# Kernel tuning notes

Hardware: AMD Instinct MI355X
Metric: run time of the kernel (lower is better)

## Reference

```python
import jax, jax.numpy as jnp
import numpy as np

N, D, H, DH = 8192, 512, 8, 64          # seq len, model dim, heads, head dim
NF = int(DH * math_log) if False else 266  # nb_features = int(64 * ln(64)) = 266
EPS = 1e-4                               # performer softmax-kernel eps
LN_EPS = 1e-5


def layernorm(x, g, b):
    mu = x.mean(-1, keepdims=True)
    var = ((x - mu) ** 2).mean(-1, keepdims=True)
    return (x - mu) * jax.lax.rsqrt(var + LN_EPS) * g + b


def softmax_kernel(data, proj, is_query):
    # data: [b,h,n,dh], proj: [nf,dh] -> phi(data): [b,h,n,nf]
    dnorm = DH ** -0.25
    ratio = NF ** -0.5
    dd = jnp.einsum('bhnd,jd->bhnj', data * dnorm, proj)
    diag = (data ** 2).sum(-1, keepdims=True) * 0.5 * (dnorm ** 2)
    if is_query:
        m = jnp.max(dd, axis=-1, keepdims=True)
    else:
        m = jnp.max(dd, axis=(-1, -2), keepdims=True)
    return ratio * (jnp.exp(dd - diag - m) + EPS)


def setup_inputs() -> dict:
    key = jax.random.key(0)
    ks = jax.random.split(key, 10)
    s = 0.02
    return {
        'x': jax.random.normal(ks[0], (N, D), jnp.float32),
        'proj': jax.random.normal(ks[1], (NF, DH), jnp.float32),
        'ln1_g': jnp.ones((D,), jnp.float32), 'ln1_b': jnp.zeros((D,), jnp.float32),
        'wq': jax.random.normal(ks[2], (D, D), jnp.float32) * s,
        'wk': jax.random.normal(ks[3], (D, D), jnp.float32) * s,
        'wv': jax.random.normal(ks[4], (D, D), jnp.float32) * s,
        'wo': jax.random.normal(ks[5], (D, D), jnp.float32) * s,
        'wo_b': jnp.zeros((D,), jnp.float32),
        'ln2_g': jnp.ones((D,), jnp.float32), 'ln2_b': jnp.zeros((D,), jnp.float32),
        'w1': jax.random.normal(ks[6], (D, 4 * D), jnp.float32) * s,
        'b1': jnp.zeros((4 * D,), jnp.float32),
        'w2': jax.random.normal(ks[7], (4 * D, D), jnp.float32) * s,
        'b2': jnp.zeros((D,), jnp.float32),
    }


def reference(x, proj, ln1_g, ln1_b, wq, wk, wv, wo, wo_b, ln2_g, ln2_b, w1, b1, w2, b2):
    xb = x[None]                                     # [1,N,D] (the unsqueeze(0))
    # --- PreLN FAVOR+ self-attention ---
    h = layernorm(xb, ln1_g, ln1_b)
    def split_heads(t):
        return t.reshape(1, N, H, DH).transpose(0, 2, 1, 3)   # [1,H,N,DH]
    q = split_heads(h @ wq)
    k = split_heads(h @ wk)
    v = split_heads(h @ wv)
    qp = softmax_kernel(q, proj, True)               # [1,H,N,NF]
    kp = softmax_kernel(k, proj, False)              # [1,H,N,NF]
    # non-causal linear attention
    context = jnp.einsum('bhnj,bhnd->bhjd', kp, v)   # [1,H,NF,DH]
    d_inv = 1.0 / jnp.einsum('bhnj,bhj->bhn', qp, kp.sum(axis=2))
    attn = jnp.einsum('bhnj,bhjd->bhnd', qp, context) * d_inv[..., None]
    attn = attn.transpose(0, 2, 1, 3).reshape(1, N, D)
    xb = xb + attn @ wo + wo_b
    # --- PreLN feed-forward (GELU, mult=4) ---
    h2 = layernorm(xb, ln2_g, ln2_b)
    xb = xb + jax.nn.gelu(h2 @ w1 + b1) @ w2 + b2
    return xb[0]                                     # squeeze -> [N,D]
```

## Files before the change

### kernel.cpp

```cpp
#include <hip/hip_runtime.h>
#include <math.h>


typedef __attribute__((ext_vector_type(8))) short bf16x8;
typedef __attribute__((ext_vector_type(4))) float f32x4;

#define N_SEQ 8192
#define DMODEL 512
#define DQKV 1536
#define NHEAD 8
#define DHEAD 64
#define NF 266
#define NFP 320
#define PEPS 1e-4f
#define LNEPS 1e-5f
#define RATIO 0.06131393694f

__device__ __forceinline__ unsigned short f2bf(float f) {
  unsigned u = __float_as_uint(f);
  u += 0x7FFFu + ((u >> 16) & 1u);
  return (unsigned short)(u >> 16);
}
__device__ __forceinline__ float bf2f(unsigned short b) {
  return __uint_as_float(((unsigned)b) << 16);
}
__device__ __forceinline__ unsigned enc_f32(float f) {
  unsigned i = __float_as_uint(f);
  return (i & 0x80000000u) ? ~i : (i | 0x80000000u);
}
__device__ __forceinline__ float dec_f32(unsigned u) {
  return (u & 0x80000000u) ? __uint_as_float(u & 0x7FFFFFFFu) : __uint_as_float(~u);
}

__device__ __forceinline__ void g2l16(const void* g, void* l) {
  __builtin_amdgcn_global_load_lds(
      (const __attribute__((address_space(1))) void*)g,
      (__attribute__((address_space(3))) void*)l, 16, 0, 0);
}

template <int N>
__device__ __forceinline__ void wait_vmcnt() {
  if constexpr (N == 0) asm volatile("s_waitcnt vmcnt(0)" ::: "memory");
  else if constexpr (N == 8) asm volatile("s_waitcnt vmcnt(8)" ::: "memory");
}
__device__ __forceinline__ void wait_lgkm0() {
  asm volatile("s_waitcnt lgkmcnt(0)" ::: "memory");
}


__global__ __launch_bounds__(256) void prep_kernel(
    const float* __restrict__ wq, const float* __restrict__ wk,
    const float* __restrict__ wv, const float* __restrict__ wo,
    const float* __restrict__ w1, const float* __restrict__ w2,
    const float* __restrict__ proj,
    unsigned short* __restrict__ wtqkv, unsigned short* __restrict__ wot,
    unsigned short* __restrict__ w1t, unsigned short* __restrict__ w2t,
    unsigned short* __restrict__ pb, unsigned* __restrict__ mk) {
  int bid = blockIdx.x;
  if (bid < 3072) {
    const float* src; unsigned short* dst; int R, C, base;
    if (bid < 256)       { src = wq; dst = wtqkv;          R = 512;  C = 512;  base = 0; }
    else if (bid < 512)  { src = wk; dst = wtqkv + 262144; R = 512;  C = 512;  base = 256; }
    else if (bid < 768)  { src = wv; dst = wtqkv + 524288; R = 512;  C = 512;  base = 512; }
    else if (bid < 1024) { src = wo; dst = wot;            R = 512;  C = 512;  base = 768; }
    else if (bid < 2048) { src = w1; dst = w1t;            R = 512;  C = 2048; base = 1024; }
    else                 { src = w2; dst = w2t;            R = 2048; C = 512;  base = 2048; }
    int lb = bid - base;
    int nbx = C / 32;
    int c0 = (lb % nbx) * 32, r0 = (lb / nbx) * 32;
    __shared__ float tile[32][33];
    int tx = threadIdx.x & 31, ty = threadIdx.x >> 5;
    #pragma unroll
    for (int i = ty; i < 32; i += 8)
      tile[i][tx] = src[(long)(r0 + i) * C + c0 + tx];
    __syncthreads();
    #pragma unroll
    for (int i = ty; i < 32; i += 8)
      dst[(long)(c0 + i) * R + r0 + tx] = f2bf(tile[tx][i]);
  } else if (bid < 3152) {
    int id = (bid - 3072) * 256 + threadIdx.x;
    int j = id >> 6;
    pb[id] = (j < NF) ? f2bf(proj[(long)j * 64 + (id & 63)] * 0.35355339059327373f)
                      : (unsigned short)0;
  } else {
    if (threadIdx.x < NHEAD) mk[threadIdx.x] = 0x007FFFFFu;
  }
}


__global__ __launch_bounds__(256) void ln_kernel(const float* __restrict__ x,
                                                 const float* __restrict__ g,
                                                 const float* __restrict__ b,
                                                 unsigned short* __restrict__ out) {
  __shared__ float sred[4];
  int row = blockIdx.x, t = threadIdx.x;
  float2 v = ((const float2*)(x + (long)row * DMODEL))[t];
  float s = v.x + v.y;
  #pragma unroll
  for (int m = 32; m >= 1; m >>= 1) s += __shfl_xor(s, m);
  if ((t & 63) == 0) sred[t >> 6] = s;
  __syncthreads();
  float mu = (sred[0] + sred[1] + sred[2] + sred[3]) * (1.0f / DMODEL);
  __syncthreads();
  float d0 = v.x - mu, d1 = v.y - mu;
  float q = d0 * d0 + d1 * d1;
  #pragma unroll
  for (int m = 32; m >= 1; m >>= 1) q += __shfl_xor(q, m);
  if ((t & 63) == 0) sred[t >> 6] = q;
  __syncthreads();
  float var = (sred[0] + sred[1] + sred[2] + sred[3]) * (1.0f / DMODEL);
  float inv = rsqrtf(var + LNEPS);
  int c = t * 2;
  unsigned short o0 = f2bf(d0 * inv * g[c] + b[c]);
  unsigned short o1 = f2bf(d1 * inv * g[c + 1] + b[c + 1]);
  ((unsigned*)(out + (long)row * DMODEL))[t] = ((unsigned)o1 << 16) | o0;
}

enum { EPI_BF16 = 0, EPI_BIAS_RES_F32 = 2, EPI_BIAS_GELU = 3, EPI_QKV = 4 };


template <int EPI>
__global__ __launch_bounds__(512, 1) void gemm8p_kernel(
    const unsigned short* __restrict__ A, int lda,
    const unsigned short* __restrict__ Bt, int ldb,
    void* __restrict__ Cv, int ldc,
    int K,
    const float* __restrict__ bias,
    unsigned short* __restrict__ vt) {
  constexpr int MR = 8, NR = 4;
  const int tid = threadIdx.x;
  const int wave = tid >> 6, lane = tid & 63;
  const int lr = lane & 15, lg = lane >> 4;
  const int wr = wave >> 2, wc = wave & 3;
  const int m0 = blockIdx.x * 256, n0 = blockIdx.y * 256;

  __shared__ uint4 a_s[2][2048];
  __shared__ uint4 b_s[2][2048];

  const unsigned short* asrc[4];
  const unsigned short* bsrc[4];
  #pragma unroll
  for (int e = 0; e < 4; ++e) {
    int chunk = e * 512 + tid;
    int r = chunk >> 3, c = chunk & 7;
    asrc[e] = A + (long)(m0 + r) * lda + (c ^ (r & 7)) * 8;
    bsrc[e] = Bt + (long)(n0 + r) * ldb + (c ^ (r & 7)) * 8;
  }
  const int wbase = tid & 448;

  f32x4 acc[MR][NR] = {};

  auto stage_a = [&](int buf, int t) {
    #pragma unroll
    for (int e = 0; e < 4; ++e)
      g2l16(asrc[e] + t * 64, &a_s[buf][e * 512 + wbase]);
  };
  auto stage_b = [&](int buf, int t) {
    #pragma unroll
    for (int e = 0; e < 4; ++e)
      g2l16(bsrc[e] + t * 64, &b_s[buf][e * 512 + wbase]);
  };
  auto compute_ks = [&](int buf, int ks) {
    bf16x8 af[MR], bv[NR];
    #pragma unroll
    for (int i = 0; i < MR; ++i) {
      int r = wr * 128 + i * 16 + lr;
      af[i] = *(const bf16x8*)&a_s[buf][r * 8 + ((ks * 4 + lg) ^ (r & 7))];
    }
    #pragma unroll
    for (int j = 0; j < NR; ++j) {
      int r = wc * 64 + j * 16 + lr;
      bv[j] = *(const bf16x8*)&b_s[buf][r * 8 + ((ks * 4 + lg) ^ (r & 7))];
    }
    __builtin_amdgcn_s_setprio(1);
    #pragma unroll
    for (int i = 0; i < MR; ++i)
      #pragma unroll
      for (int j = 0; j < NR; ++j)
        acc[i][j] = __builtin_amdgcn_mfma_f32_16x16x32_bf16(af[i], bv[j], acc[i][j], 0, 0, 0);
    __builtin_amdgcn_s_setprio(0);
  };

  const int NT = K >> 6;
  stage_a(0, 0);
  stage_b(0, 0);
  wait_vmcnt<0>();
  __builtin_amdgcn_s_barrier();

  for (int t = 0; t < NT; ++t) {
    const int cur = t & 1;
    const bool more = (t + 1 < NT);
    if (more) stage_a(cur ^ 1, t + 1);
    compute_ks(cur, 0);
    if (more) stage_b(cur ^ 1, t + 1);
    compute_ks(cur, 1);
    if (more) {
      wait_lgkm0();
      __builtin_amdgcn_sched_barrier(0);
      __builtin_amdgcn_s_barrier();
      wait_vmcnt<0>();
      __builtin_amdgcn_s_barrier();
    }
  }

  #pragma unroll
  for (int i = 0; i < MR; ++i) {
    #pragma unroll
    for (int j = 0; j < NR; ++j) {
      int gn = n0 + wc * 64 + j * 16 + lr;
      int gm0 = m0 + wr * 128 + i * 16 + lg * 4;
      if (EPI == EPI_QKV && gn >= 1024) {
        int d = gn - 1024;
        uint2 u;
        u.x = (unsigned)f2bf(acc[i][j][0]) | ((unsigned)f2bf(acc[i][j][1]) << 16);
        u.y = (unsigned)f2bf(acc[i][j][2]) | ((unsigned)f2bf(acc[i][j][3]) << 16);
        *(uint2*)(vt + (long)d * N_SEQ + gm0) = u;
        continue;
      }
      #pragma unroll
      for (int rg = 0; rg < 4; ++rg) {
        int gm = gm0 + rg;
        float v = acc[i][j][rg];
        if (EPI == EPI_BF16 || EPI == EPI_QKV) {
          ((unsigned short*)Cv)[(long)gm * ldc + gn] = f2bf(v);
        } else if (EPI == EPI_BIAS_GELU) {
          v += bias[gn];
          float t3 = 0.7978845608028654f * (v + 0.044715f * v * v * v);
          v = v / (1.0f + __expf(-2.0f * t3));
          ((unsigned short*)Cv)[(long)gm * ldc + gn] = f2bf(v);
        }
      }
    }
  }
}


template <int BM, int BN, int WM, int WN, int EPI>
__global__ __launch_bounds__(256) void gemm_kernel(
    const unsigned short* __restrict__ A, int lda,
    const unsigned short* __restrict__ Bt, int ldb,
    void* __restrict__ Cv, int ldc,
    int K,
    const float* __restrict__ bias,
    const float* __restrict__ res, int ldr) {
  static_assert((BM / WM) * (BN / WN) == 4, "need 4 waves");
  constexpr int MR = WM / 16, NR = WN / 16;
  constexpr int WNN = BN / WN;
  constexpr int AIT = BM * 8 / 256;
  constexpr int BIT = BN * 8 / 256;
  const int tid = threadIdx.x;
  const int wave = tid >> 6, lane = tid & 63;
  const int lr = lane & 15, lg = lane >> 4;
  const int wr = wave / WNN, wc = wave % WNN;
  const int m0 = blockIdx.x * BM, n0 = blockIdx.y * BN;

  __shared__ uint4 a_s[2][BM * 8];
  __shared__ uint4 b_s[2][BN * 8];

  const unsigned short* asrc[AIT];
  #pragma unroll
  for (int e = 0; e < AIT; ++e) {
    int chunk = e * 256 + tid;
    int r = chunk >> 3, c = chunk & 7;
    asrc[e] = A + (long)(m0 + r) * lda + (c ^ (r & 7)) * 8;
  }
  const unsigned short* bsrc[BIT];
  #pragma unroll
  for (int e = 0; e < BIT; ++e) {
    int chunk = e * 256 + tid;
    int r = chunk >> 3, c = chunk & 7;
    bsrc[e] = Bt + (long)(n0 + r) * ldb + (c ^ (r & 7)) * 8;
  }
  const int wbase = tid & 192;

  f32x4 acc[MR][NR] = {};

  auto stage = [&](int buf, int t) {
    #pragma unroll
    for (int e = 0; e < AIT; ++e)
      g2l16(asrc[e] + t * 64, &a_s[buf][e * 256 + wbase]);
    #pragma unroll
    for (int e = 0; e < BIT; ++e)
      g2l16(bsrc[e] + t * 64, &b_s[buf][e * 256 + wbase]);
  };
  auto compute = [&](int buf) {
    #pragma unroll
    for (int ks = 0; ks < 2; ++ks) {
      bf16x8 af[MR], bv[NR];
      #pragma unroll
      for (int i = 0; i < MR; ++i) {
        int r = wr * WM + i * 16 + lr;
        af[i] = *(const bf16x8*)&a_s[buf][r * 8 + ((ks * 4 + lg) ^ (r & 7))];
      }
      #pragma unroll
      for (int j = 0; j < NR; ++j) {
        int r = wc * WN + j * 16 + lr;
        bv[j] = *(const bf16x8*)&b_s[buf][r * 8 + ((ks * 4 + lg) ^ (r & 7))];
      }
      #pragma unroll
      for (int i = 0; i < MR; ++i)
        #pragma unroll
        for (int j = 0; j < NR; ++j)
          acc[i][j] = __builtin_amdgcn_mfma_f32_16x16x32_bf16(af[i], bv[j], acc[i][j], 0, 0, 0);
    }
  };

  const int NT = K >> 6;
  stage(0, 0);
  stage(1, 1);
  wait_vmcnt<8>();
  __builtin_amdgcn_s_barrier();

  int cur = 0;
  for (int t = 0; t < NT; ++t) {
    compute(cur);
    if (t + 1 < NT) {
      wait_lgkm0();
      __builtin_amdgcn_s_barrier();
      if (t + 2 < NT) {
        stage(cur, t + 2);
        wait_vmcnt<8>();
      } else {
        wait_vmcnt<0>();
      }
      __builtin_amdgcn_s_barrier();
    }
    cur ^= 1;
  }

  #pragma unroll
  for (int i = 0; i < MR; ++i) {
    #pragma unroll
    for (int j = 0; j < NR; ++j) {
      int gn = n0 + wc * WN + j * 16 + lr;
      #pragma unroll
      for (int rg = 0; rg < 4; ++rg) {
        int gm = m0 + wr * WM + i * 16 + lg * 4 + rg;
        float v = acc[i][j][rg];
        if (EPI == EPI_BF16) {
          ((unsigned short*)Cv)[(long)gm * ldc + gn] = f2bf(v);
        } else if (EPI == EPI_BIAS_RES_F32) {
          v += bias[gn] + res[(long)gm * ldr + gn];
          ((float*)Cv)[(long)gm * ldc + gn] = v;
        } else if (EPI == EPI_BIAS_GELU) {
          v += bias[gn];
          float t3 = 0.7978845608028654f * (v + 0.044715f * v * v * v);
          v = v / (1.0f + __expf(-2.0f * t3));
          ((unsigned short*)Cv)[(long)gm * ldc + gn] = f2bf(v);
        }
      }
    }
  }
}


__global__ __launch_bounds__(256) void kmax_kernel(
    const unsigned short* __restrict__ Kp,
    const unsigned short* __restrict__ pb,
    unsigned* __restrict__ mk) {
  const int tid = threadIdx.x;
  const int wave = tid >> 6, lane = tid & 63;
  const int lr = lane & 15, lg = lane >> 4;
  const int h = blockIdx.z;
  const int m0 = blockIdx.x * 64;

  __shared__ uint4 a_s4[512];
  __shared__ uint4 b_s4[2560];
  __shared__ float sred[4];

  const unsigned short* Aq = Kp + (long)m0 * DQKV + h * DHEAD;
  const int wbase = tid & 192;

  #pragma unroll
  for (int e = 0; e < 2; ++e) {
    int chunk = e * 256 + tid;
    int r = chunk >> 3, c = chunk & 7;
    g2l16(Aq + (long)r * DQKV + (c ^ (r & 7)) * 8, a_s4 + e * 256 + wbase);
  }
  #pragma unroll
  for (int e = 0; e < 10; ++e) {
    int chunk = e * 256 + tid;
    int r = chunk >> 3, c = chunk & 7;
    g2l16(pb + (long)r * DHEAD + (c ^ (r & 7)) * 8, b_s4 + e * 256 + wbase);
  }
  __syncthreads();

  f32x4 acc[17] = {};
  #pragma unroll
  for (int ks = 0; ks < 2; ++ks) {
    int rA = wave * 16 + lr;
    bf16x8 af = *(const bf16x8*)&a_s4[rA * 8 + ((ks * 4 + lg) ^ (rA & 7))];
    #pragma unroll
    for (int j = 0; j < 17; ++j) {
      int rB = j * 16 + lr;
      bf16x8 bv = *(const bf16x8*)&b_s4[rB * 8 + ((ks * 4 + lg) ^ (rB & 7))];
      acc[j] = __builtin_amdgcn_mfma_f32_16x16x32_bf16(af, bv, acc[j], 0, 0, 0);
    }
  }

  float m = -3.0e38f;
  #pragma unroll
  for (int j = 0; j < 17; ++j) {
    bool valid = (j < 16) || (lr < 10);
    if (valid) {
      #pragma unroll
      for (int rg = 0; rg < 4; ++rg) m = fmaxf(m, acc[j][rg]);
    }
  }
  #pragma unroll
  for (int s = 1; s < 64; s <<= 1) m = fmaxf(m, __shfl_xor(m, s));
  if (lane == 0) sred[wave] = m;
  __syncthreads();
  if (tid == 0) {
    float mm = fmaxf(fmaxf(sred[0], sred[1]), fmaxf(sred[2], sred[3]));
    atomicMax(&mk[h], enc_f32(mm));
  }
}


__global__ __launch_bounds__(256) void ctx_fused_kernel(
    const unsigned short* __restrict__ Kp,
    const unsigned short* __restrict__ pb,
    const unsigned short* __restrict__ vT,
    const unsigned* __restrict__ mk,
    float* __restrict__ part,
    float* __restrict__ kspart) {
  const int tid = threadIdx.x;
  const int wave = tid >> 6, lane = tid & 63;
  const int lr = lane & 15, lg = lane >> 4;
  const int kc = blockIdx.x, h = blockIdx.y;
  const int wbase = tid & 192;

  __shared__ uint4 smem[7168];
  uint4* pbs = smem;
  auto kbuf = [&](int b) { return smem + 2560 + b * 512; };
  auto vbuf = [&](int b) { return smem + 3584 + b * 512; };
  uint4* Pt = smem + 4608;

  #pragma unroll
  for (int e = 0; e < 10; ++e) {
    int chunk = e * 256 + tid;
    int r = chunk >> 3, c = chunk & 7;
    g2l16(pb + (long)r * DHEAD + (c ^ (r & 7)) * 8, pbs + e * 256 + wbase);
  }

  auto stage_kv = [&](int b, int sub) {
    int n0 = kc * 256 + sub * 64;
    #pragma unroll
    for (int e = 0; e < 2; ++e) {
      int chunk = e * 256 + tid;
      int r = chunk >> 3, c = chunk & 7;
      g2l16(Kp + (long)(n0 + r) * DQKV + h * DHEAD + (c ^ (r & 7)) * 8,
            kbuf(b) + e * 256 + wbase);
      g2l16(vT + ((long)h * DHEAD + r) * N_SEQ + n0 + (c ^ (r & 7)) * 8,
            vbuf(b) + e * 256 + wbase);
    }
  };

  const float mh = dec_f32(mk[h]);
  f32x4 acc2[2][10] = {};
  float colacc[20];
  #pragma unroll
  for (int j = 0; j < 20; ++j) colacc[j] = 0.f;

  const int wr = wave >> 1, wc = wave & 1;

  stage_kv(0, 0);
  for (int sub = 0; sub < 4; ++sub) {
    const int cur = sub & 1;
    __syncthreads();
    if (sub + 1 < 4) stage_kv(cur ^ 1, sub + 1);

    f32x4 acc[20] = {};
    float qs = 0.f;
    #pragma unroll
    for (int ks = 0; ks < 2; ++ks) {
      int rA = wave * 16 + lr;
      bf16x8 af = *(const bf16x8*)&kbuf(cur)[rA * 8 + ((ks * 4 + lg) ^ (rA & 7))];
      #pragma unroll
      for (int i = 0; i < 8; ++i) {
        float f = bf2f((unsigned short)af[i]);
        qs += f * f;
      }
      #pragma unroll
      for (int j = 0; j < 20; ++j) {
        int rB = j * 16 + lr;
        bf16x8 bv = *(const bf16x8*)&pbs[rB * 8 + ((ks * 4 + lg) ^ (rB & 7))];
        acc[j] = __builtin_amdgcn_mfma_f32_16x16x32_bf16(af, bv, acc[j], 0, 0, 0);
      }
    }
    qs += __shfl_xor(qs, 16);
    qs += __shfl_xor(qs, 32);
    float dg[4];
    #pragma unroll
    for (int rg = 0; rg < 4; ++rg) dg[rg] = 0.0625f * __shfl(qs, lg * 4 + rg);

    __syncthreads();

    unsigned short* Ptu = (unsigned short*)Pt;
    const int nrow = wave * 16 + lg * 4;
    #pragma unroll
    for (int j = 0; j < 20; ++j) {
      int colj = j * 16 + lr;
      #pragma unroll
      for (int rg = 0; rg < 4; ++rg) {
        float v = 0.f;
        if (colj < NF) v = RATIO * (__expf(acc[j][rg] - dg[rg] - mh) + PEPS);
        colacc[j] += v;
        int nr = nrow + rg;
        int idx = ((colj * 8 + ((nr >> 3) ^ (colj & 7))) << 3) + (nr & 7);
        Ptu[idx] = f2bf(v);
      }
    }
    __syncthreads();

    #pragma unroll
    for (int ks = 0; ks < 2; ++ks) {
      bf16x8 af[2], bv[10];
      #pragma unroll
      for (int i = 0; i < 2; ++i) {
        int r = wr * 32 + i * 16 + lr;
        af[i] = *(const bf16x8*)&vbuf(cur)[r * 8 + ((ks * 4 + lg) ^ (r & 7))];
      }
      #pragma unroll
      for (int j = 0; j < 10; ++j) {
        int r = wc * 160 + j * 16 + lr;
        bv[j] = *(const bf16x8*)&Pt[r * 8 + ((ks * 4 + lg) ^ (r & 7))];
      }
      #pragma unroll
      for (int i = 0; i < 2; ++i)
        #pragma unroll
        for (int j = 0; j < 10; ++j)
          acc2[i][j] = __builtin_amdgcn_mfma_f32_16x16x32_bf16(af[i], bv[j], acc2[i][j], 0, 0, 0);
    }
  }

  float* pbase = part + ((long)(h * 32 + kc)) * 64 * NFP;
  #pragma unroll
  for (int i = 0; i < 2; ++i) {
    #pragma unroll
    for (int j = 0; j < 10; ++j) {
      int gn = wc * 160 + j * 16 + lr;
      #pragma unroll
      for (int rg = 0; rg < 4; ++rg) {
        int gm = wr * 32 + i * 16 + lg * 4 + rg;
        pbase[(long)gm * NFP + gn] = acc2[i][j][rg];
      }
    }
  }

  __syncthreads();
  float* kls = (float*)Pt;
  #pragma unroll
  for (int j = 0; j < 20; ++j) {
    float cs = colacc[j];
    cs += __shfl_xor(cs, 16);
    cs += __shfl_xor(cs, 32);
    if (lg == 0) kls[wave * NFP + j * 16 + lr] = cs;
  }
  __syncthreads();
  for (int c0 = tid; c0 < NFP; c0 += 256) {
    kspart[((long)(h * 32 + kc)) * NFP + c0] =
        kls[c0] + kls[NFP + c0] + kls[2 * NFP + c0] + kls[3 * NFP + c0];
  }
}


__global__ void ctx_reduce_kernel(const float* __restrict__ part,
                                  const float* __restrict__ kspart,
                                  unsigned short* __restrict__ ctxpad) {
  int i = blockIdx.x * 256 + threadIdx.x;
  int h = i / (96 * NFP);
  int rem = i % (96 * NFP);
  int r = rem / NFP, j = rem % NFP;
  float s = 0.f;
  if (r < 64) {
    #pragma unroll 4
    for (int kc = 0; kc < 32; ++kc)
      s += part[((long)(h * 32 + kc)) * 64 * NFP + r * NFP + j];
  } else if (r == 64) {
    #pragma unroll 4
    for (int kc = 0; kc < 32; ++kc)
      s += kspart[((long)(h * 32 + kc)) * NFP + j];
  }
  ctxpad[i] = f2bf(s);
}


__global__ __launch_bounds__(256) void attn_fused_kernel(
    const unsigned short* __restrict__ Qp,
    const unsigned short* __restrict__ pb,
    const unsigned short* __restrict__ ctxpad,
    unsigned short* __restrict__ attn) {
  const int tid = threadIdx.x;
  const int wave = tid >> 6, lane = tid & 63;
  const int lr = lane & 15, lg = lane >> 4;
  const int h = blockIdx.z;
  const int m0 = blockIdx.x * 64;
  const int wbase = tid & 192;

  __shared__ uint4 smem[4096];
  auto sbuf = [&](int b) { return smem + b * 768; };
  uint4* Pf = smem + 1536;

  const unsigned short* Aq = Qp + (long)m0 * DQKV + h * DHEAD;
  const unsigned short* Ch = ctxpad + (long)h * 96 * NFP;

  auto stage_ctx = [&](int b, int kk) {
    #pragma unroll
    for (int e = 0; e < 3; ++e) {
      int chunk = e * 256 + tid;
      int r = chunk >> 3, c = chunk & 7;
      g2l16(Ch + (long)r * NFP + kk * 64 + (c ^ (r & 7)) * 8, sbuf(b) + e * 256 + wbase);
    }
  };

  #pragma unroll
  for (int e = 0; e < 2; ++e) {
    int chunk = e * 256 + tid;
    int r = chunk >> 3, c = chunk & 7;
    g2l16(Aq + (long)r * DQKV + (c ^ (r & 7)) * 8, sbuf(0) + e * 256 + wbase);
  }
  #pragma unroll
  for (int e = 0; e < 10; ++e) {
    int chunk = e * 256 + tid;
    int r = chunk >> 3, c = chunk & 7;
    g2l16(pb + (long)r * DHEAD + (c ^ (r & 7)) * 8, Pf + e * 256 + wbase);
  }
  __syncthreads();

  f32x4 acc[20] = {};
  float qs = 0.f;
  #pragma unroll
  for (int ks = 0; ks < 2; ++ks) {
    int rA = wave * 16 + lr;
    bf16x8 af = *(const bf16x8*)&sbuf(0)[rA * 8 + ((ks * 4 + lg) ^ (rA & 7))];
    #pragma unroll
    for (int i = 0; i < 8; ++i) {
      float f = bf2f((unsigned short)af[i]);
      qs += f * f;
    }
    #pragma unroll
    for (int j = 0; j < 20; ++j) {
      int rB = j * 16 + lr;
      bf16x8 bv = *(const bf16x8*)&Pf[rB * 8 + ((ks * 4 + lg) ^ (rB & 7))];
      acc[j] = __builtin_amdgcn_mfma_f32_16x16x32_bf16(af, bv, acc[j], 0, 0, 0);
    }
  }
  qs += __shfl_xor(qs, 16);
  qs += __shfl_xor(qs, 32);
  float dg[4];
  #pragma unroll
  for (int rg = 0; rg < 4; ++rg) dg[rg] = 0.0625f * __shfl(qs, lg * 4 + rg);

  float mrow[4];
  #pragma unroll
  for (int rg = 0; rg < 4; ++rg) mrow[rg] = -3.0e38f;
  #pragma unroll
  for (int j = 0; j < 17; ++j) {
    bool valid = (j < 16) || (lr < 10);
    if (valid) {
      #pragma unroll
      for (int rg = 0; rg < 4; ++rg) mrow[rg] = fmaxf(mrow[rg], acc[j][rg]);
    }
  }
  #pragma unroll
  for (int s = 1; s < 16; s <<= 1)
    #pragma unroll
    for (int rg = 0; rg < 4; ++rg) mrow[rg] = fmaxf(mrow[rg], __shfl_xor(mrow[rg], s));

  __syncthreads();
  stage_ctx(0, 0);

  unsigned short* Pu = (unsigned short*)Pf;
  const int prow = wave * 16 + lg * 4;
  #pragma unroll
  for (int j = 0; j < 20; ++j) {
    int col = j * 16 + lr;
    int kk = col >> 6, cc = (col >> 3) & 7;
    #pragma unroll
    for (int rg = 0; rg < 4; ++rg) {
      float v = 0.f;
      if (col < NF) v = RATIO * (__expf(acc[j][rg] - dg[rg] - mrow[rg]) + PEPS);
      int rw = prow + rg;
      int idx = ((kk * 512 + rw * 8 + (cc ^ (rw & 7))) << 3) + (col & 7);
      Pu[idx] = f2bf(v);
    }
  }
  __syncthreads();

  f32x4 acc2[6] = {};
  #pragma unroll
  for (int kk = 0; kk < 5; ++kk) {
    const int cur = kk & 1;
    if (kk + 1 < 5) stage_ctx(cur ^ 1, kk + 1);
    #pragma unroll
    for (int ks = 0; ks < 2; ++ks) {
      int rA = wave * 16 + lr;
      bf16x8 af = *(const bf16x8*)&Pf[kk * 512 + rA * 8 + ((ks * 4 + lg) ^ (rA & 7))];
      #pragma unroll
      for (int j = 0; j < 6; ++j) {
        int rB = j * 16 + lr;
        bf16x8 bv = *(const bf16x8*)&sbuf(cur)[rB * 8 + ((ks * 4 + lg) ^ (rB & 7))];
        acc2[j] = __builtin_amdgcn_mfma_f32_16x16x32_bf16(af, bv, acc2[j], 0, 0, 0);
      }
    }
    if (kk + 1 < 5) __syncthreads();
  }

  #pragma unroll
  for (int rg = 0; rg < 4; ++rg) {
    float dv = __shfl(acc2[4][rg], lane & 48);
    float inv = 1.0f / dv;
    int gm = m0 + wave * 16 + lg * 4 + rg;
    #pragma unroll
    for (int j = 0; j < 4; ++j) {
      attn[(long)gm * DMODEL + h * DHEAD + j * 16 + lr] = f2bf(acc2[j][rg] * inv);
    }
  }
}


extern "C" void kernel_launch(void* const* d_in, const int* in_sizes, int n_in,
                              void* d_out, int out_size, void* d_ws, size_t ws_size,
                              hipStream_t stream) {
  const float* x    = (const float*)d_in[0];
  const float* proj = (const float*)d_in[1];
  const float* ln1g = (const float*)d_in[2];
  const float* ln1b = (const float*)d_in[3];
  const float* wq   = (const float*)d_in[4];
  const float* wk   = (const float*)d_in[5];
  const float* wv   = (const float*)d_in[6];
  const float* wo   = (const float*)d_in[7];
  const float* wob  = (const float*)d_in[8];
  const float* ln2g = (const float*)d_in[9];
  const float* ln2b = (const float*)d_in[10];
  const float* w1   = (const float*)d_in[11];
  const float* b1   = (const float*)d_in[12];
  const float* w2   = (const float*)d_in[13];
  const float* b2   = (const float*)d_in[14];

  char* ws = (char*)d_ws;
  unsigned short* wtqkv = (unsigned short*)(ws + 0);
  unsigned short* wot   = (unsigned short*)(ws + 1572864);
  unsigned short* w1t   = (unsigned short*)(ws + 2097152);
  unsigned short* w2t   = (unsigned short*)(ws + 4194304);
  unsigned short* pb    = (unsigned short*)(ws + 6291456);
  unsigned short* h_bf  = (unsigned short*)(ws + 6332416);
  unsigned short* qkv   = (unsigned short*)(ws + 14721024);
  unsigned* mk          = (unsigned*)(ws + 124297216);
  unsigned short* vT    = (unsigned short*)(ws + 124297472);
  float* part           = (float*)(ws + 132686080);
  float* kspart         = (float*)(ws + 153657600);
  unsigned short* ctxpad= (unsigned short*)(ws + 154978560);
  unsigned short* gbf   = (unsigned short*)(ws + 130468096);
  unsigned short* attn  = h_bf;
  unsigned short* h2    = qkv;
  float* xb             = (float*)d_out;

  dim3 blk(256);

  prep_kernel<<<3153, blk, 0, stream>>>(wq, wk, wv, wo, w1, w2, proj,
                                        wtqkv, wot, w1t, w2t, pb, mk);

  ln_kernel<<<N_SEQ, blk, 0, stream>>>(x, ln1g, ln1b, h_bf);

  gemm8p_kernel<EPI_QKV><<<dim3(32, 6), dim3(512), 0, stream>>>(
      h_bf, 512, wtqkv, 512, qkv, DQKV, 512, nullptr, vT);

  kmax_kernel<<<dim3(128, 1, 8), blk, 0, stream>>>(qkv + 512, pb, mk);

  ctx_fused_kernel<<<dim3(32, 8), blk, 0, stream>>>(qkv + 512, pb, vT, mk, part, kspart);
  ctx_reduce_kernel<<<960, blk, 0, stream>>>(part, kspart, ctxpad);

  attn_fused_kernel<<<dim3(128, 1, 8), blk, 0, stream>>>(qkv, pb, ctxpad, attn);

  gemm_kernel<128, 64, 64, 32, EPI_BIAS_RES_F32><<<dim3(64, 8), blk, 0, stream>>>(
      attn, 512, wot, 512, xb, 512, 512, wob, x, 512);

  ln_kernel<<<N_SEQ, blk, 0, stream>>>(xb, ln2g, ln2b, h2);

  gemm8p_kernel<EPI_BIAS_GELU><<<dim3(32, 8), dim3(512), 0, stream>>>(
      h2, 512, w1t, 512, gbf, 2048, 512, b1, nullptr);

  gemm_kernel<128, 64, 64, 32, EPI_BIAS_RES_F32><<<dim3(64, 8), blk, 0, stream>>>(
      gbf, 2048, w2t, 2048, d_out, 512, 2048, b2, xb, 512);
}
```

Baseline: 188.1 us.

## Retile GEMMs to 256x64 blocks with multi-stage prefetch and fuse LN1 into prep

Result: faster. 179.8 us (-4.4%).

```diff
diff --git a/kernel.cpp b/kernel.cpp
--- a/kernel.cpp
+++ b/kernel.cpp
@@ -41,7 +41,8 @@
 template <int N>
 __device__ __forceinline__ void wait_vmcnt() {
   if constexpr (N == 0) asm volatile("s_waitcnt vmcnt(0)" ::: "memory");
-  else if constexpr (N == 8) asm volatile("s_waitcnt vmcnt(8)" ::: "memory");
+  else if constexpr (N == 5) asm volatile("s_waitcnt vmcnt(5)" ::: "memory");
+  else if constexpr (N == 6) asm volatile("s_waitcnt vmcnt(6)" ::: "memory");
 }
 __device__ __forceinline__ void wait_lgkm0() {
   asm volatile("s_waitcnt lgkmcnt(0)" ::: "memory");
@@ -55,7 +56,10 @@
     const float* __restrict__ proj,
     unsigned short* __restrict__ wtqkv, unsigned short* __restrict__ wot,
     unsigned short* __restrict__ w1t, unsigned short* __restrict__ w2t,
-    unsigned short* __restrict__ pb, unsigned* __restrict__ mk) {
+    unsigned short* __restrict__ pb, unsigned* __restrict__ mk,
+    const float* __restrict__ x,
+    const float* __restrict__ ln1g, const float* __restrict__ ln1b,
+    unsigned short* __restrict__ h_bf) {
   int bid = blockIdx.x;
   if (bid < 3072) {
     const float* src; unsigned short* dst; int R, C, base;
@@ -82,8 +86,31 @@
     int j = id >> 6;
     pb[id] = (j < NF) ? f2bf(proj[(long)j * 64 + (id & 63)] * 0.35355339059327373f)
                       : (unsigned short)0;
+  } else if (bid == 3152) {
+    if (threadIdx.x < NHEAD) mk[threadIdx.x] = 0x007FFFFFu;
   } else {
-    if (threadIdx.x < NHEAD) mk[threadIdx.x] = 0x007FFFFFu;
+    __shared__ float sred[4];
+    int row = bid - 3153, t = threadIdx.x;
+    float2 v = ((const float2*)(x + (long)row * DMODEL))[t];
+    float s = v.x + v.y;
+    #pragma unroll
+    for (int m = 32; m >= 1; m >>= 1) s += __shfl_xor(s, m);
+    if ((t & 63) == 0) sred[t >> 6] = s;
+    __syncthreads();
+    float mu = (sred[0] + sred[1] + sred[2] + sred[3]) * (1.0f / DMODEL);
+    __syncthreads();
+    float d0 = v.x - mu, d1 = v.y - mu;
+    float q = d0 * d0 + d1 * d1;
+    #pragma unroll
+    for (int m = 32; m >= 1; m >>= 1) q += __shfl_xor(q, m);
+    if ((t & 63) == 0) sred[t >> 6] = q;
+    __syncthreads();
+    float var = (sred[0] + sred[1] + sred[2] + sred[3]) * (1.0f / DMODEL);
+    float inv = rsqrtf(var + LNEPS);
+    int c = t * 2;
+    unsigned short o0 = f2bf(d0 * inv * ln1g[c] + ln1b[c]);
+    unsigned short o1 = f2bf(d1 * inv * ln1g[c + 1] + ln1b[c + 1]);
+    ((unsigned*)(h_bf + (long)row * DMODEL))[t] = ((unsigned)o1 << 16) | o0;
   }
 }
 
@@ -120,95 +147,98 @@
 
 
 template <int EPI>
-__global__ __launch_bounds__(512, 1) void gemm8p_kernel(
+__global__ __launch_bounds__(512, 4) void gemm8w_kernel(
     const unsigned short* __restrict__ A, int lda,
     const unsigned short* __restrict__ Bt, int ldb,
     void* __restrict__ Cv, int ldc,
     int K,
     const float* __restrict__ bias,
+    const float* __restrict__ res, int ldr,
     unsigned short* __restrict__ vt) {
-  constexpr int MR = 8, NR = 4;
+  constexpr int MR = 4, NR = 2;
+  constexpr int S = 5;
   const int tid = threadIdx.x;
   const int wave = tid >> 6, lane = tid & 63;
   const int lr = lane & 15, lg = lane >> 4;
-  const int wr = wave >> 2, wc = wave & 3;
-  const int m0 = blockIdx.x * 256, n0 = blockIdx.y * 256;
+  const int wr = wave >> 1, wc = wave & 1;
+  const int m0 = blockIdx.x * 256, n0 = blockIdx.y * 64;
 
   __shared__ uint4 a_s[2][2048];
-  __shared__ uint4 b_s[2][2048];
+  __shared__ uint4 b_s[2][512];
 
   const unsigned short* asrc[4];
-  const unsigned short* bsrc[4];
   #pragma unroll
   for (int e = 0; e < 4; ++e) {
     int chunk = e * 512 + tid;
     int r = chunk >> 3, c = chunk & 7;
     asrc[e] = A + (long)(m0 + r) * lda + (c ^ (r & 7)) * 8;
-    bsrc[e] = Bt + (long)(n0 + r) * ldb + (c ^ (r & 7)) * 8;
+  }
+  const unsigned short* bsrc;
+  {
+    int r = tid >> 3, c = tid & 7;
+    bsrc = Bt + (long)(n0 + r) * ldb + (c ^ (r & 7)) * 8;
   }
   const int wbase = tid & 448;
 
   f32x4 acc[MR][NR] = {};
 
-  auto stage_a = [&](int buf, int t) {
+  auto stage = [&](int buf, int t) {
     #pragma unroll
     for (int e = 0; e < 4; ++e)
       g2l16(asrc[e] + t * 64, &a_s[buf][e * 512 + wbase]);
+    g2l16(bsrc + t * 64, &b_s[buf][wbase]);
   };
-  auto stage_b = [&](int buf, int t) {
-    #pragma unroll
-    for (int e = 0; e < 4; ++e)
-      g2l16(bsrc[e] + t * 64, &b_s[buf][e * 512 + wbase]);
+  auto compute = [&](int buf) {
+    #pragma unroll
+    for (int ks = 0; ks < 2; ++ks) {
+      bf16x8 af[MR], bv[NR];
+      #pragma unroll
+      for (int i = 0; i < MR; ++i) {
+        int r = wr * 64 + i * 16 + lr;
+        af[i] = *(const bf16x8*)&a_s[buf][r * 8 + ((ks * 4 + lg) ^ (r & 7))];
+      }
+      #pragma unroll
+      for (int j = 0; j < NR; ++j) {
+        int r = wc * 32 + j * 16 + lr;
+        bv[j] = *(const bf16x8*)&b_s[buf][r * 8 + ((ks * 4 + lg) ^ (r & 7))];
+      }
+      #pragma unroll
+      for (int i = 0; i < MR; ++i)
+        #pragma unroll
+        for (int j = 0; j < NR; ++j)
+          acc[i][j] = __builtin_amdgcn_mfma_f32_16x16x32_bf16(af[i], bv[j], acc[i][j], 0, 0, 0);
+    }
   };
-  auto compute_ks = [&](int buf, int ks) {
-    bf16x8 af[MR], bv[NR];
-    #pragma unroll
-    for (int i = 0; i < MR; ++i) {
-      int r = wr * 128 + i * 16 + lr;
-      af[i] = *(const bf16x8*)&a_s[buf][r * 8 + ((ks * 4 + lg) ^ (r & 7))];
-    }
+
+  const int NT = K >> 6;
+  stage(0, 0);
+  stage(1, 1);
+  wait_vmcnt<S>();
+  __builtin_amdgcn_s_barrier();
+
+  int cur = 0;
+  for (int t = 0; t < NT; ++t) {
+    compute(cur);
+    if (t + 1 < NT) {
+      wait_lgkm0();
+      __builtin_amdgcn_s_barrier();
+      if (t + 2 < NT) {
+        stage(cur, t + 2);
+        wait_vmcnt<S>();
+      } else {
+        wait_vmcnt<0>();
+      }
+      __builtin_amdgcn_s_barrier();
+    }
+    cur ^= 1;
+  }
+
+  #pragma unroll
+  for (int i = 0; i < MR; ++i) {
     #pragma unroll
     for (int j = 0; j < NR; ++j) {
-      int r = wc * 64 + j * 16 + lr;
-      bv[j] = *(const bf16x8*)&b_s[buf][r * 8 + ((ks * 4 + lg) ^ (r & 7))];
-    }
-    __builtin_amdgcn_s_setprio(1);
-    #pragma unroll
-    for (int i = 0; i < MR; ++i)
-      #pragma unroll
-      for (int j = 0; j < NR; ++j)
-        acc[i][j] = __builtin_amdgcn_mfma_f32_16x16x32_bf16(af[i], bv[j], acc[i][j], 0, 0, 0);
-    __builtin_amdgcn_s_setprio(0);
-  };
-
-  const int NT = K >> 6;
-  stage_a(0, 0);
-  stage_b(0, 0);
-  wait_vmcnt<0>();
-  __builtin_amdgcn_s_barrier();
-
-  for (int t = 0; t < NT; ++t) {
-    const int cur = t & 1;
-    const bool more = (t + 1 < NT);
-    if (more) stage_a(cur ^ 1, t + 1);
-    compute_ks(cur, 0);
-    if (more) stage_b(cur ^ 1, t + 1);
-    compute_ks(cur, 1);
-    if (more) {
-      wait_lgkm0();
-      __builtin_amdgcn_sched_barrier(0);
-      __builtin_amdgcn_s_barrier();
-      wait_vmcnt<0>();
-      __builtin_amdgcn_s_barrier();
-    }
-  }
-
-  #pragma unroll
-  for (int i = 0; i < MR; ++i) {
-    #pragma unroll
-    for (int j = 0; j < NR; ++j) {
-      int gn = n0 + wc * 64 + j * 16 + lr;
-      int gm0 = m0 + wr * 128 + i * 16 + lg * 4;
+      int gn = n0 + wc * 32 + j * 16 + lr;
+      int gm0 = m0 + wr * 64 + i * 16 + lg * 4;
       if (EPI == EPI_QKV && gn >= 1024) {
         int d = gn - 1024;
         uint2 u;
@@ -223,6 +253,9 @@
         float v = acc[i][j][rg];
         if (EPI == EPI_BF16 || EPI == EPI_QKV) {
           ((unsigned short*)Cv)[(long)gm * ldc + gn] = f2bf(v);
+        } else if (EPI == EPI_BIAS_RES_F32) {
+          v += bias[gn] + res[(long)gm * ldr + gn];
+          ((float*)Cv)[(long)gm * ldc + gn] = v;
         } else if (EPI == EPI_BIAS_GELU) {
           v += bias[gn];
           float t3 = 0.7978845608028654f * (v + 0.044715f * v * v * v);
@@ -248,6 +281,8 @@
   constexpr int WNN = BN / WN;
   constexpr int AIT = BM * 8 / 256;
   constexpr int BIT = BN * 8 / 256;
+  constexpr int S = AIT + BIT;
+  static_assert(S == 6, "wait count tuned for BM=128,BN=64");
   const int tid = threadIdx.x;
   const int wave = tid >> 6, lane = tid & 63;
   const int lr = lane & 15, lg = lane >> 4;
@@ -308,7 +343,7 @@
   const int NT = K >> 6;
   stage(0, 0);
   stage(1, 1);
-  wait_vmcnt<8>();
+  wait_vmcnt<6>();
   __builtin_amdgcn_s_barrier();
 
   int cur = 0;
@@ -319,7 +354,7 @@
       __builtin_amdgcn_s_barrier();
       if (t + 2 < NT) {
         stage(cur, t + 2);
-        wait_vmcnt<8>();
+        wait_vmcnt<6>();
       } else {
         wait_vmcnt<0>();
       }
@@ -362,51 +397,60 @@
   const int wave = tid >> 6, lane = tid & 63;
   const int lr = lane & 15, lg = lane >> 4;
   const int h = blockIdx.z;
-  const int m0 = blockIdx.x * 64;
-
-  __shared__ uint4 a_s4[512];
-  __shared__ uint4 b_s4[2560];
+  const int m0 = blockIdx.x * 256;
+  const int wbase = tid & 192;
+
+  __shared__ uint4 pbs[2560];
+  __shared__ uint4 abuf[2][512];
   __shared__ float sred[4];
 
-  const unsigned short* Aq = Kp + (long)m0 * DQKV + h * DHEAD;
-  const int wbase = tid & 192;
-
-  #pragma unroll
-  for (int e = 0; e < 2; ++e) {
-    int chunk = e * 256 + tid;
-    int r = chunk >> 3, c = chunk & 7;
-    g2l16(Aq + (long)r * DQKV + (c ^ (r & 7)) * 8, a_s4 + e * 256 + wbase);
-  }
   #pragma unroll
   for (int e = 0; e < 10; ++e) {
     int chunk = e * 256 + tid;
     int r = chunk >> 3, c = chunk & 7;
-    g2l16(pb + (long)r * DHEAD + (c ^ (r & 7)) * 8, b_s4 + e * 256 + wbase);
-  }
-  __syncthreads();
-
-  f32x4 acc[17] = {};
-  #pragma unroll
-  for (int ks = 0; ks < 2; ++ks) {
-    int rA = wave * 16 + lr;
-    bf16x8 af = *(const bf16x8*)&a_s4[rA * 8 + ((ks * 4 + lg) ^ (rA & 7))];
+    g2l16(pb + (long)r * DHEAD + (c ^ (r & 7)) * 8, pbs + e * 256 + wbase);
+  }
+  auto stage_a = [&](int b, int sub) {
+    #pragma unroll
+    for (int e = 0; e < 2; ++e) {
+      int chunk = e * 256 + tid;
+      int r = chunk >> 3, c = chunk & 7;
+      g2l16(Kp + (long)(m0 + sub * 64 + r) * DQKV + h * DHEAD + (c ^ (r & 7)) * 8,
+            abuf[b] + e * 256 + wbase);
+    }
+  };
+
+  stage_a(0, 0);
+  __syncthreads();
+
+  float m = -3.0e38f;
+  for (int sub = 0; sub < 4; ++sub) {
+    const int cur = sub & 1;
+    if (sub + 1 < 4) stage_a(cur ^ 1, sub + 1);
+
+    f32x4 acc[17] = {};
+    #pragma unroll
+    for (int ks = 0; ks < 2; ++ks) {
+      int rA = wave * 16 + lr;
+      bf16x8 af = *(const bf16x8*)&abuf[cur][rA * 8 + ((ks * 4 + lg) ^ (rA & 7))];
+      #pragma unroll
+      for (int j = 0; j < 17; ++j) {
+        int rB = j * 16 + lr;
+        bf16x8 bv = *(const bf16x8*)&pbs[rB * 8 + ((ks * 4 + lg) ^ (rB & 7))];
+        acc[j] = __builtin_amdgcn_mfma_f32_16x16x32_bf16(af, bv, acc[j], 0, 0, 0);
+      }
+    }
     #pragma unroll
     for (int j = 0; j < 17; ++j) {
-      int rB = j * 16 + lr;
-      bf16x8 bv = *(const bf16x8*)&b_s4[rB * 8 + ((ks * 4 + lg) ^ (rB & 7))];
-      acc[j] = __builtin_amdgcn_mfma_f32_16x16x32_bf16(af, bv, acc[j], 0, 0, 0);
-    }
-  }
-
-  float m = -3.0e38f;
-  #pragma unroll
-  for (int j = 0; j < 17; ++j) {
-    bool valid = (j < 16) || (lr < 10);
-    if (valid) {
-      #pragma unroll
-      for (int rg = 0; rg < 4; ++rg) m = fmaxf(m, acc[j][rg]);
-    }
-  }
+      bool valid = (j < 16) || (lr < 10);
+      if (valid) {
+        #pragma unroll
+        for (int rg = 0; rg < 4; ++rg) m = fmaxf(m, acc[j][rg]);
+      }
+    }
+    if (sub + 1 < 4) __syncthreads();
+  }
+
   #pragma unroll
   for (int s = 1; s < 64; s <<= 1) m = fmaxf(m, __shfl_xor(m, s));
   if (lane == 0) sred[wave] = m;
@@ -760,15 +804,14 @@
 
   dim3 blk(256);
 
-  prep_kernel<<<3153, blk, 0, stream>>>(wq, wk, wv, wo, w1, w2, proj,
-                                        wtqkv, wot, w1t, w2t, pb, mk);
-
-  ln_kernel<<<N_SEQ, blk, 0, stream>>>(x, ln1g, ln1b, h_bf);
-
-  gemm8p_kernel<EPI_QKV><<<dim3(32, 6), dim3(512), 0, stream>>>(
-      h_bf, 512, wtqkv, 512, qkv, DQKV, 512, nullptr, vT);
-
-  kmax_kernel<<<dim3(128, 1, 8), blk, 0, stream>>>(qkv + 512, pb, mk);
+  prep_kernel<<<11345, blk, 0, stream>>>(wq, wk, wv, wo, w1, w2, proj,
+                                         wtqkv, wot, w1t, w2t, pb, mk,
+                                         x, ln1g, ln1b, h_bf);
+
+  gemm8w_kernel<EPI_QKV><<<dim3(32, 24), dim3(512), 0, stream>>>(
+      h_bf, 512, wtqkv, 512, qkv, DQKV, 512, nullptr, nullptr, 0, vT);
+
+  kmax_kernel<<<dim3(32, 1, 8), blk, 0, stream>>>(qkv + 512, pb, mk);
 
   ctx_fused_kernel<<<dim3(32, 8), blk, 0, stream>>>(qkv + 512, pb, vT, mk, part, kspart);
   ctx_reduce_kernel<<<960, blk, 0, stream>>>(part, kspart, ctxpad);
@@ -780,9 +823,9 @@
 
   ln_kernel<<<N_SEQ, blk, 0, stream>>>(xb, ln2g, ln2b, h2);
 
-  gemm8p_kernel<EPI_BIAS_GELU><<<dim3(32, 8), dim3(512), 0, stream>>>(
-      h2, 512, w1t, 512, gbf, 2048, 512, b1, nullptr);
-
-  gemm_kernel<128, 64, 64, 32, EPI_BIAS_RES_F32><<<dim3(64, 8), blk, 0, stream>>>(
-      gbf, 2048, w2t, 2048, d_out, 512, 2048, b2, xb, 512);
-}
+  gemm8w_kernel<EPI_BIAS_GELU><<<dim3(32, 32), dim3(512), 0, stream>>>(
+      h2, 512, w1t, 512, gbf, 2048, 512, b1, nullptr, 0, nullptr);
+
+  gemm8w_kernel<EPI_BIAS_RES_F32><<<dim3(32, 8), dim3(512), 0, stream>>>(
+      gbf, 2048, w2t, 2048, d_out, 512, 2048, b2, xb, 512, nullptr);
+}
```
